# Performance work log

Hardware: AMD Instinct MI355X
Metric: run time of the kernel (lower is better)

Reference implementation:

```python
import jax, jax.numpy as jnp
import numpy as np

B, T, OB = 64, 512, 256
H = 1024
AC = 8
EPS = 1e-6


def rmsnorm(x, scale):
    # RMSNorm over the last (hidden) dim with learned scale
    return x * scale * jax.lax.rsqrt(jnp.mean(x * x, axis=-1, keepdims=True) + EPS)


def lstm_layer(x, Wih, Whh, b, gnorm, cnorm):
    """RMSNorm-gated LSTM layer. x: [B,T,in] -> [B,T,H].
    Gate pre-activations are RMSNorm'd per-gate; cell state is RMSNorm'd
    before the output tanh (the norm that breaks cuDNN gate fusion)."""
    Bsz = x.shape[0]
    Hh = Whh.shape[1]
    # precompute input projection for all timesteps: [B,T,4H]
    xp = jnp.einsum('bti,gi->btg', x, Wih) + b

    def step(carry, xpt):
        h, c = carry
        z = xpt + h @ Whh.T  # [B,4H]
        zi, zf, zg, zo = jnp.split(z, 4, axis=-1)
        i = jax.nn.sigmoid(rmsnorm(zi, gnorm[0]))
        f = jax.nn.sigmoid(rmsnorm(zf, gnorm[1]))
        g = jnp.tanh(rmsnorm(zg, gnorm[2]))
        o = jax.nn.sigmoid(rmsnorm(zo, gnorm[3]))
        c = f * c + i * g
        h = o * jnp.tanh(rmsnorm(c, cnorm))
        return (h, c), h

    init = (jnp.zeros((Bsz, Hh), x.dtype), jnp.zeros((Bsz, Hh), x.dtype))
    _, hs = jax.lax.scan(step, init, jnp.swapaxes(xp, 0, 1))  # [T,B,H]
    return jnp.swapaxes(hs, 0, 1)


def setup_inputs() -> dict:
    key = jax.random.key(0)
    ks = jax.random.split(key, 12)

    def w(k, shape, fan_in):
        return jax.random.normal(k, shape, dtype=jnp.float32) / np.sqrt(fan_in)

    return {
        'obs': jax.random.normal(ks[0], (B, T, OB), dtype=jnp.float32),
        'Wih0': w(ks[1], (4 * H, OB), OB),
        'Whh0': w(ks[2], (4 * H, H), H),
        'b0': jnp.zeros((4 * H,), jnp.float32),
        'gnorm0': jnp.ones((4, H), jnp.float32),
        'cnorm0': jnp.ones((H,), jnp.float32),
        'Wih1': w(ks[3], (4 * H, H), H),
        'Whh1': w(ks[4], (4 * H, H), H),
        'b1': jnp.zeros((4 * H,), jnp.float32),
        'gnorm1': jnp.ones((4, H), jnp.float32),
        'cnorm1': jnp.ones((H,), jnp.float32),
        'Wout': w(ks[5], (AC, H), H),
        'bout': jnp.zeros((AC,), jnp.float32),
        'std_param': jnp.zeros((AC,), jnp.float32),
    }


def reference(obs, Wih0, Whh0, b0, gnorm0, cnorm0,
              Wih1, Whh1, b1, gnorm1, cnorm1,
              Wout, bout, std_param):
    out = lstm_layer(obs, Wih0, Whh0, b0, gnorm0, cnorm0)
    out = lstm_layer(out, Wih1, Whh1, b1, gnorm1, cnorm1)
    features = out[:, -1, :]              # last timestep, like out[:, -1, :]
    mean = features @ Wout.T + bout       # [B, AC]
    std = jax.nn.softplus(std_param) + 0.01  # global learned std, [AC]
    return mean, std
```

## Files before the change

### kernel.cpp

```cpp
#include <hip/hip_runtime.h>
#include <hip/hip_bf16.h>

typedef __attribute__((ext_vector_type(8))) __bf16 bf16x8;
typedef __attribute__((ext_vector_type(4))) float f32x4;
typedef unsigned short u16;
typedef unsigned int u32;
typedef unsigned long long u64;

#define NB 64
#define NT 512
#define NH 1024
#define NOB 256
#define NWG 256
#define G4H 4096
#define BH (NB*NH)

#define S_OBS 0
#define S_H0  16384
#define S_H1  81920
#define LDS_TOTAL 147456

#define KT0 10
#define KT1 16

#define AS_RELAXED __ATOMIC_RELAXED
#define SCOPE_AGENT __HIP_MEMORY_SCOPE_AGENT
#define KEEPW(x) asm volatile("" : "+v"(x))

#define SBAR  do { asm volatile("s_barrier" ::: "memory"); __builtin_amdgcn_sched_barrier(0); } while (0)
#define LGKM0 do { asm volatile("s_waitcnt lgkmcnt(0)" ::: "memory"); __builtin_amdgcn_sched_barrier(0); } while (0)
#define VMW0  do { asm volatile("s_waitcnt vmcnt(0)" ::: "memory"); __builtin_amdgcn_sched_barrier(0); } while (0)
#define VMW8  do { asm volatile("s_waitcnt vmcnt(8)" ::: "memory"); __builtin_amdgcn_sched_barrier(0); } while (0)

__device__ __forceinline__ u16 f2bf(float f) {
  __hip_bfloat16 h = __float2bfloat16(f);
  return *reinterpret_cast<u16*>(&h);
}
__device__ __forceinline__ float sigm(float x) { return 1.f / (1.f + __expf(-x)); }
__device__ __forceinline__ float tanh_f(float x) {
  float e = __expf(2.f * x);
  return 1.f - 2.f / (e + 1.f);
}

__device__ __forceinline__ void gload_lds16(const void* g, void* l) {
  __builtin_amdgcn_global_load_lds(
      (const __attribute__((address_space(1))) void*)g,
      (__attribute__((address_space(3))) void*)l, 16, 0, 0);
}

__device__ __forceinline__ int4 load_b128_coh(const void* p) {
  int4 v;
  asm volatile("global_load_dwordx4 %0, %1, off sc0 sc1\n\ts_waitcnt vmcnt(0)"
               : "=v"(v) : "v"(p) : "memory");
  return v;
}
__device__ __forceinline__ u64 AL64(const u64* p) {
  return __hip_atomic_load(p, AS_RELAXED, SCOPE_AGENT);
}

__device__ __forceinline__ void gridbar(int* bar, int gen, bool wait) {
  __syncthreads();
  if (threadIdx.x < 64) {
    const int lane = threadIdx.x;
    if (lane == 0)
      __hip_atomic_fetch_add(&bar[(blockIdx.x & 15) * 32], 1, AS_RELAXED, SCOPE_AGENT);
    if (wait) {
      const int tgt = NWG * gen;
      for (;;) {
        int v = (lane < 16)
              ? __hip_atomic_load(&bar[lane * 32], AS_RELAXED, SCOPE_AGENT) : 0;
#pragma unroll
        for (int off = 8; off; off >>= 1) v += __shfl_xor(v, off);
        v = __shfl(v, 0);
        if (v >= tgt) break;
        __builtin_amdgcn_s_sleep(1);
      }
    }
  }
  __syncthreads();
}

__device__ __host__ __forceinline__ int wavek0(int kq, int kt) {
  return kt < 2 ? kq * 64 + kt * 32 : 256 + kq * 256 + (kt - 2) * 32;
}
__device__ __host__ __forceinline__ int wavek1(int kq, int kt) {
  return kq * 512 + kt * 32;
}

template<int LAYER>
__global__ void __launch_bounds__(256)
pack_weights(const float* __restrict__ Wih, const float* __restrict__ Whh,
             u16* __restrict__ wp) {
  constexpr int KT = LAYER ? KT1 : KT0;
  constexpr int KIN = LAYER ? 1024 : 256;
  const int total = 128 * 2 * 4 * KT * 64;
  for (int idx = blockIdx.x * blockDim.x + threadIdx.x; idx < total;
       idx += gridDim.x * blockDim.x) {
    int lane = idx & 63;
    int q = idx >> 6;
    int kt = q % KT; q /= KT;
    int kq = q & 3; q >>= 2;
    int nt = q & 1; q >>= 1;
    int slice = q;
    int outr = slice * 32 + nt * 16 + (lane & 15);
    int kb = (LAYER ? wavek1(kq, kt) : wavek0(kq, kt)) + (lane >> 4) * 8;
    union { u16 uu[8]; int4 qv; } vv;
#pragma unroll
    for (int j = 0; j < 8; ++j) {
      int k = kb + j;
      float f = (k < KIN) ? Wih[(long)outr * KIN + k] : Whh[(long)outr * NH + (k - KIN)];
      vv.uu[j] = f2bf(f);
    }
    reinterpret_cast<int4*>(wp)[idx] = vv.qv;
  }
}

__global__ void __launch_bounds__(256)
transpose_obs(const float* __restrict__ obs, u16* __restrict__ obsT) {
  long idx = (long)blockIdx.x * blockDim.x + threadIdx.x;
  if (idx >= (long)NT * NB * NOB) return;
  int k = (int)(idx & (NOB - 1));
  long r = idx >> 8;
  int b = (int)(r & (NB - 1));
  int t = (int)(r >> 6);
  obsT[idx] = f2bf(obs[((long)b * NT + t) * NOB + k]);
}

template<bool H1COH>
__global__ void __launch_bounds__(512)
fused_lstm(const u16* __restrict__ obsT,
           const u16* __restrict__ wp0, const u16* __restrict__ wp1,
           const float* __restrict__ b0, const float* __restrict__ gn0,
           const float* __restrict__ cn0,
           const float* __restrict__ b1, const float* __restrict__ gn1,
           const float* __restrict__ cn1,
           u16* __restrict__ h0hist, u16* __restrict__ h1buf, long long h1step,
           float* __restrict__ zbuf, float* __restrict__ feat,
           int* __restrict__ bar) {
  extern __shared__ char smem[];
  f32x4* sred = reinterpret_cast<f32x4*>(smem + S_H1);
  float* p2red = reinterpret_cast<float*>(smem + S_H0);

  const int tid = threadIdx.x;
  const int lane = tid & 63;
  const int wave = tid >> 6;
  const int nt = wave & 1;
  const int kq = wave >> 1;
  const int col = lane & 15;
  const int rgrp = lane >> 4;
  const int wg = blockIdx.x;
  const int bg = wg >> 7;
  const int slice = wg & 127;
  const int kl = (wave & 1) * 64 + lane;
  const int w2 = wave >> 1;

  bf16x8 wf0[KT0], wf1[KT1];
  {
    const bf16x8* p0 = reinterpret_cast<const bf16x8*>(wp0)
                     + ((size_t)((slice * 2 + nt) * 4 + kq) * KT0) * 64 + lane;
#pragma unroll
    for (int u = 0; u < KT0; ++u) { wf0[u] = p0[u * 64]; KEEPW(wf0[u]); }
    const bf16x8* p1 = reinterpret_cast<const bf16x8*>(wp1)
                     + ((size_t)((slice * 2 + nt) * 4 + kq) * KT1) * 64 + lane;
#pragma unroll
    for (int u = 0; u < KT1; ++u) { wf1[u] = p1[u * 64]; KEEPW(wf1[u]); }
  }

  const int l2 = (wg >> 6) & 1;
  const int prow = wg & 63;
  const int ej = tid * 2;
  float gn[8];
  float cw0 = 0.f, cw1 = 0.f;
  float c0 = 0.f, c1 = 0.f;
  if (wg < 128) {
    const float* gnp = l2 ? gn1 : gn0;
    const float* cnp = l2 ? cn1 : cn0;
#pragma unroll
    for (int g = 0; g < 4; ++g) {
      gn[g * 2]     = gnp[g * NH + ej];
      gn[g * 2 + 1] = gnp[g * NH + ej + 1];
    }
    cw0 = cnp[ej];
    cw1 = cnp[ej + 1];
  }
  constexpr float inv = 1.f / 1024.f;
  const bool p2wg = (wg < 128);

  {
    const u16* os = obsT + (size_t)(bg * 32) * NOB;
#pragma unroll
    for (int i = 0; i < 2; ++i) {
      const int row = 16 * i + 2 * wave + (lane >> 5);
      gload_lds16(os + (size_t)row * NOB + (size_t)(((lane & 31) ^ (row & 7)) * 8),
                  smem + S_OBS + (i * 512 + wave * 64) * 16);
    }
  }

  int gen = 0;

  for (int r = 0; r <= NT; ++r) {
    const u16* h0s = h0hist + (size_t)r * BH + (size_t)(bg * 32) * NH;
    const u16* h1s = h1buf + (size_t)r * h1step + (size_t)(bg * 32) * NH;
#pragma unroll
    for (int i = 0; i < 8; ++i) {
      const int row = i * 4 + w2;
      const int koff = (kl ^ (row & 7)) * 8;
      gload_lds16(h0s + (size_t)row * NH + koff,
                  smem + S_H0 + (i * 512 + wave * 64) * 16);
    }
    if constexpr (!H1COH) {
#pragma unroll
      for (int i = 0; i < 8; ++i) {
        const int row = i * 4 + w2;
        const int koff = (kl ^ (row & 7)) * 8;
        gload_lds16(h1s + (size_t)row * NH + koff,
                    smem + S_H1 + (i * 512 + wave * 64) * 16);
      }
      VMW8;
      SBAR;
    } else {
#pragma unroll 1
      for (int c = tid; c < 4096; c += 512) {
        int row = c >> 7, kc = c & 127;
        int4 v = load_b128_coh(h1s + (size_t)row * NH + kc * 8);
        *reinterpret_cast<int4*>(smem + S_H1 + row * 2048 + ((kc ^ (row & 7)) << 4)) = v;
      }
      VMW0; LGKM0;
      SBAR;
    }

    f32x4 a00 = {0,0,0,0}, a01 = {0,0,0,0};
    f32x4 a10 = {0,0,0,0}, a11 = {0,0,0,0};
    if (r < NT) {
#pragma unroll
      for (int kt = 0; kt < KT0; ++kt) {
        const int base   = (kt < 2) ? S_OBS : S_H0;
        const int rowstr = (kt < 2) ? 512 : 2048;
        const int chunk0 = (kt < 2) ? (kq * 8 + kt * 4) : (kq * 32 + (kt - 2) * 4);
        const int sw = (((chunk0 + rgrp) ^ (col & 7)) << 4);
        bf16x8 am0 = *reinterpret_cast<const bf16x8*>(smem + base + col * rowstr + sw);
        bf16x8 am1 = *reinterpret_cast<const bf16x8*>(smem + base + (16 + col) * rowstr + sw);
        a00 = __builtin_amdgcn_mfma_f32_16x16x32_bf16(am0, wf0[kt], a00, 0, 0, 0);
        a01 = __builtin_amdgcn_mfma_f32_16x16x32_bf16(am1, wf0[kt], a01, 0, 0, 0);
      }
    }
    if constexpr (!H1COH) {
      VMW0;
      SBAR;
    }

    if (r >= 1) {
      const int base = (kq < 2) ? S_H0 : S_H1;
#pragma unroll
      for (int kt = 0; kt < KT1; ++kt) {
        const int chunk0 = (kq & 1) * 64 + kt * 4;
        const int sw = (((chunk0 + rgrp) ^ (col & 7)) << 4);
        bf16x8 am0 = *reinterpret_cast<const bf16x8*>(smem + base + col * 2048 + sw);
        bf16x8 am1 = *reinterpret_cast<const bf16x8*>(smem + base + (16 + col) * 2048 + sw);
        a10 = __builtin_amdgcn_mfma_f32_16x16x32_bf16(am0, wf1[kt], a10, 0, 0, 0);
        a11 = __builtin_amdgcn_mfma_f32_16x16x32_bf16(am1, wf1[kt], a11, 0, 0, 0);
      }
    }
    LGKM0;
    SBAR;

    {
      f32x4* pw = sred + wave * 512 + lane;
      pw[0 * 64] = a00;
      pw[1 * 64] = a01;
      pw[2 * 64] = a10;
      pw[3 * 64] = a11;
    }
    LGKM0;
    SBAR;
    {
      const int q = tid >> 6, ln = tid & 63;
      const int fcol = ln & 15, frg = ln >> 4;
      const int lm = q & 3;
      const int nq2 = q >> 2;
      f32x4 s = sred[(nq2 + 0) * 512 + lm * 64 + ln]
              + sred[(nq2 + 2) * 512 + lm * 64 + ln]
              + sred[(nq2 + 4) * 512 + lm * 64 + ln]
              + sred[(nq2 + 6) * 512 + lm * 64 + ln];
      const int l = lm >> 1, m = lm & 1;
      const bool zv = l ? (r >= 1) : (r < NT);
      if (zv) {
        const int outg = slice * 32 + nq2 * 16 + fcol;
        const float bv = (l ? b1 : b0)[outg];
        float* zr = zbuf + ((size_t)l * NB + bg * 32 + m * 16 + frg * 4) * G4H + outg;
#pragma unroll
        for (int j = 0; j < 4; ++j)
          __hip_atomic_store(&zr[(size_t)j * G4H], s[j] + bv, AS_RELAXED, SCOPE_AGENT);
      }
    }
    gridbar(bar, ++gen, p2wg);

    if (r + 1 < NT) {
      const u16* os = obsT + (size_t)(r + 1) * (NB * NOB) + (size_t)(bg * 32) * NOB;
#pragma unroll
      for (int i = 0; i < 2; ++i) {
        const int row = 16 * i + 2 * wave + (lane >> 5);
        gload_lds16(os + (size_t)row * NOB + (size_t)(((lane & 31) ^ (row & 7)) * 8),
                    smem + S_OBS + (i * 512 + wave * 64) * 16);
      }
    }

    if (p2wg && (l2 ? (r >= 1) : (r < NT))) {
      const u64* zq = reinterpret_cast<const u64*>(
          zbuf + ((size_t)l2 * NB + prow) * G4H);
      union { u64 q; float f[2]; } va, vb, vg, vo;
      va.q = AL64(zq + tid);
      vb.q = AL64(zq + 512 + tid);
      vg.q = AL64(zq + 1024 + tid);
      vo.q = AL64(zq + 1536 + tid);
      float s0 = va.f[0] * va.f[0] + va.f[1] * va.f[1];
      float s1 = vb.f[0] * vb.f[0] + vb.f[1] * vb.f[1];
      float s2 = vg.f[0] * vg.f[0] + vg.f[1] * vg.f[1];
      float s3 = vo.f[0] * vo.f[0] + vo.f[1] * vo.f[1];
#pragma unroll
      for (int off = 32; off; off >>= 1) {
        s0 += __shfl_xor(s0, off);
        s1 += __shfl_xor(s1, off);
        s2 += __shfl_xor(s2, off);
        s3 += __shfl_xor(s3, off);
      }
      if (lane == 0) {
        float* sp = p2red + wave * 4;
        sp[0] = s0; sp[1] = s1; sp[2] = s2; sp[3] = s3;
      }
      __syncthreads();
      float t0 = 0.f, t1 = 0.f, t2 = 0.f, t3 = 0.f;
#pragma unroll
      for (int w = 0; w < 8; ++w) {
        t0 += p2red[w * 4 + 0]; t1 += p2red[w * 4 + 1];
        t2 += p2red[w * 4 + 2]; t3 += p2red[w * 4 + 3];
      }
      const float r0 = rsqrtf(t0 * inv + 1e-6f);
      const float r1 = rsqrtf(t1 * inv + 1e-6f);
      const float r2 = rsqrtf(t2 * inv + 1e-6f);
      const float r3 = rsqrtf(t3 * inv + 1e-6f);
      const float i0 = sigm(va.f[0] * gn[0] * r0), i1 = sigm(va.f[1] * gn[1] * r0);
      const float f0 = sigm(vb.f[0] * gn[2] * r1), f1 = sigm(vb.f[1] * gn[3] * r1);
      const float g0 = tanh_f(vg.f[0] * gn[4] * r2), g1 = tanh_f(vg.f[1] * gn[5] * r2);
      const float o0 = sigm(vo.f[0] * gn[6] * r3), o1 = sigm(vo.f[1] * gn[7] * r3);
      c0 = f0 * c0 + i0 * g0;
      c1 = f1 * c1 + i1 * g1;
      float cs = c0 * c0 + c1 * c1;
#pragma unroll
      for (int off = 32; off; off >>= 1) cs += __shfl_xor(cs, off);
      if (lane == 0) p2red[32 + wave] = cs;
      __syncthreads();
      float ct = 0.f;
#pragma unroll
      for (int w = 0; w < 8; ++w) ct += p2red[32 + w];
      const float rc = rsqrtf(ct * inv + 1e-6f);
      const float hx = o0 * tanh_f(c0 * cw0 * rc);
      const float hy = o1 * tanh_f(c1 * cw1 * rc);
      u16* hw;
      if (l2 == 0) hw = h0hist + (size_t)(r + 1) * BH + (size_t)prow * NH + ej;
      else         hw = h1buf + (size_t)(r + 1) * h1step + (size_t)prow * NH + ej;
      const u32 packed = (u32)f2bf(hx) | ((u32)f2bf(hy) << 16);
      __hip_atomic_store(reinterpret_cast<u32*>(hw), packed, AS_RELAXED, SCOPE_AGENT);
      if (l2 == 1 && r == NT) {
        feat[(size_t)prow * NH + ej] = hx;
        feat[(size_t)prow * NH + ej + 1] = hy;
      }
    }
    gridbar(bar, ++gen, true);
  }
}

__global__ void __launch_bounds__(256)
head_kernel(const float* __restrict__ feat, const float* __restrict__ Wout,
            const float* __restrict__ bout, const float* __restrict__ stdp,
            float* __restrict__ out) {
  int b = blockIdx.x;
  int a = threadIdx.x >> 5;
  int l = threadIdx.x & 31;
  float s = 0.f;
  for (int k = l; k < NH; k += 32) s += feat[b * NH + k] * Wout[a * NH + k];
#pragma unroll
  for (int off = 16; off; off >>= 1) s += __shfl_xor(s, off, 32);
  if (l == 0) out[b * 8 + a] = s + bout[a];
  if (b == 0 && threadIdx.x < 8) {
    float x = stdp[threadIdx.x];
    float splus = (x > 20.f) ? x : log1pf(__expf(x));
    out[512 + threadIdx.x] = splus + 0.01f;
  }
}

extern "C" void kernel_launch(void* const* d_in, const int* in_sizes, int n_in,
                              void* d_out, int out_size, void* d_ws, size_t ws_size,
                              hipStream_t stream) {
  (void)in_sizes; (void)n_in; (void)out_size;
  const float* obs  = (const float*)d_in[0];
  const float* Wih0 = (const float*)d_in[1];
  const float* Whh0 = (const float*)d_in[2];
  const float* b0   = (const float*)d_in[3];
  const float* gn0  = (const float*)d_in[4];
  const float* cn0  = (const float*)d_in[5];
  const float* Wih1 = (const float*)d_in[6];
  const float* Whh1 = (const float*)d_in[7];
  const float* b1   = (const float*)d_in[8];
  const float* gn1  = (const float*)d_in[9];
  const float* cn1  = (const float*)d_in[10];
  const float* Wout = (const float*)d_in[11];
  const float* bout = (const float*)d_in[12];
  const float* stdp = (const float*)d_in[13];
  float* out = (float*)d_out;

  char* ws = (char*)d_ws;
  size_t off = 0;
  auto take = [&](size_t bytes) -> char* {
    char* p = ws + off;
    off = (off + bytes + 255) & ~(size_t)255;
    return p;
  };

  const size_t WP0_B  = (size_t)128 * 2 * 4 * KT0 * 64 * 16;
  const size_t WP1_B  = (size_t)128 * 2 * 4 * KT1 * 64 * 16;
  const size_t OBST_B = (size_t)NT * NB * NOB * 2;
  const size_t H0H_B  = (size_t)(NT + 1) * BH * 2;
  const size_t H1H_B  = (size_t)(NT + 2) * BH * 2;

  u16* wp0    = (u16*)take(WP0_B);
  u16* wp1    = (u16*)take(WP1_B);
  u16* obsT   = (u16*)take(OBST_B);
  u16* h0hist = (u16*)take(H0H_B);
  u16* h1b    = (u16*)take(H1H_B);
  float* zbuf = (float*)take((size_t)2 * NB * G4H * 4);
  float* feat = (float*)take((size_t)NB * NH * 4);
  int* bars   = (int*)take(4096);
  bool fits = (off <= ws_size);
  long long h1step = BH;

  if (!fits) {
    off = 0;
    wp0    = (u16*)take(WP0_B);
    wp1    = (u16*)take(WP1_B);
    obsT   = (u16*)take(OBST_B);
    h0hist = (u16*)take(H0H_B);
    h1b    = (u16*)take((size_t)BH * 2);
    zbuf   = (float*)take((size_t)2 * NB * G4H * 4);
    feat   = (float*)take((size_t)NB * NH * 4);
    bars   = (int*)take(4096);
    h1step = 0;
    if (off > ws_size) return;
  }

  (void)hipFuncSetAttribute((const void*)fused_lstm<false>,
                            hipFuncAttributeMaxDynamicSharedMemorySize, LDS_TOTAL);
  (void)hipFuncSetAttribute((const void*)fused_lstm<true>,
                            hipFuncAttributeMaxDynamicSharedMemorySize, LDS_TOTAL);

  hipMemsetAsync(bars, 0, 4096, stream);
  hipMemsetAsync(h0hist, 0, (size_t)BH * 2, stream);
  hipMemsetAsync(h1b, 0, (size_t)(fits ? 2 : 1) * BH * 2, stream);

  pack_weights<0><<<2560, 256, 0, stream>>>(Wih0, Whh0, wp0);
  pack_weights<1><<<4096, 256, 0, stream>>>(Wih1, Whh1, wp1);
  transpose_obs<<<(NT * NB * NOB) / 256, 256, 0, stream>>>(obs, obsT);

  if (fits) {
    fused_lstm<false><<<NWG, 512, LDS_TOTAL, stream>>>(
        obsT, wp0, wp1, b0, gn0, cn0, b1, gn1, cn1,
        h0hist, h1b, h1step, zbuf, feat, bars);
  } else {
    fused_lstm<true><<<NWG, 512, LDS_TOTAL, stream>>>(
        obsT, wp0, wp1, b0, gn0, cn0, b1, gn1, cn1,
        h0hist, h1b, 0LL, zbuf, feat, bars);
  }

  head_kernel<<<NB, 256, 0, stream>>>(feat, Wout, bout, stdp, out);
}
```

Before: 6.455 ms.

## Split layer phases into half-steps with dedicated pointwise wave and per-batch-group barriers

The fused persistent LSTM loop is restructured into alternating half-steps: even half-steps run layer-0 GEMMs and layer-1 pointwise, odd half-steps run layer-1 GEMMs and layer-0 pointwise. A ninth wave per workgroup does the RMSNorm/gate pointwise work on 16 elements per lane, and the grid barrier is split per batch group (128 WGs each). This aims to remove the second grid barrier per step and overlap pointwise work with MFMA work. It doubles the number of loop iterations and removes the fallback path for small workspaces.

Measured after the change: 17.97 ms. 2.78x slower.

```diff
diff --git a/kernel.cpp b/kernel.cpp
--- a/kernel.cpp
+++ b/kernel.cpp
@@ -3,6 +3,7 @@
 
 typedef __attribute__((ext_vector_type(8))) __bf16 bf16x8;
 typedef __attribute__((ext_vector_type(4))) float f32x4;
+typedef __attribute__((ext_vector_type(4))) int i32x4;
 typedef unsigned short u16;
 typedef unsigned int u32;
 typedef unsigned long long u64;
@@ -12,13 +13,15 @@
 #define NH 1024
 #define NOB 256
 #define NWG 256
+#define HALF_WG 128
 #define G4H 4096
 #define BH (NB*NH)
 
 #define S_OBS 0
 #define S_H0  16384
 #define S_H1  81920
-#define LDS_TOTAL 147456
+#define S_RED 147456
+#define LDS_TOTAL 163840
 
 #define KT0 10
 #define KT1 16
@@ -30,7 +33,7 @@
 #define SBAR  do { asm volatile("s_barrier" ::: "memory"); __builtin_amdgcn_sched_barrier(0); } while (0)
 #define LGKM0 do { asm volatile("s_waitcnt lgkmcnt(0)" ::: "memory"); __builtin_amdgcn_sched_barrier(0); } while (0)
 #define VMW0  do { asm volatile("s_waitcnt vmcnt(0)" ::: "memory"); __builtin_amdgcn_sched_barrier(0); } while (0)
-#define VMW8  do { asm volatile("s_waitcnt vmcnt(8)" ::: "memory"); __builtin_amdgcn_sched_barrier(0); } while (0)
+#define VMW2  do { asm volatile("s_waitcnt vmcnt(2)" ::: "memory"); __builtin_amdgcn_sched_barrier(0); } while (0)
 
 __device__ __forceinline__ u16 f2bf(float f) {
   __hip_bfloat16 h = __float2bfloat16(f);
@@ -47,34 +50,28 @@
       (const __attribute__((address_space(1))) void*)g,
       (__attribute__((address_space(3))) void*)l, 16, 0, 0);
 }
-
-__device__ __forceinline__ int4 load_b128_coh(const void* p) {
-  int4 v;
-  asm volatile("global_load_dwordx4 %0, %1, off sc0 sc1\n\ts_waitcnt vmcnt(0)"
-               : "=v"(v) : "v"(p) : "memory");
-  return v;
-}
-__device__ __forceinline__ u64 AL64(const u64* p) {
-  return __hip_atomic_load(p, AS_RELAXED, SCOPE_AGENT);
-}
-
-__device__ __forceinline__ void gridbar(int* bar, int gen, bool wait) {
+__device__ __forceinline__ void ld16a(i32x4& d, const void* p) {
+  asm volatile("global_load_dwordx4 %0, %1, off sc0 sc1" : "=v"(d) : "v"(p));
+}
+__device__ __forceinline__ void st16c(void* p, i32x4 v) {
+  asm volatile("global_store_dwordx4 %0, %1, off sc0 sc1" :: "v"(p), "v"(v) : "memory");
+}
+
+__device__ __forceinline__ void gridbar(int* barD, int myleaf, int gen) {
   __syncthreads();
   if (threadIdx.x < 64) {
     const int lane = threadIdx.x;
     if (lane == 0)
-      __hip_atomic_fetch_add(&bar[(blockIdx.x & 15) * 32], 1, AS_RELAXED, SCOPE_AGENT);
-    if (wait) {
-      const int tgt = NWG * gen;
-      for (;;) {
-        int v = (lane < 16)
-              ? __hip_atomic_load(&bar[lane * 32], AS_RELAXED, SCOPE_AGENT) : 0;
-#pragma unroll
-        for (int off = 8; off; off >>= 1) v += __shfl_xor(v, off);
-        v = __shfl(v, 0);
-        if (v >= tgt) break;
-        __builtin_amdgcn_s_sleep(1);
-      }
+      __hip_atomic_fetch_add(&barD[myleaf * 32], 1, AS_RELAXED, SCOPE_AGENT);
+    const int tgt = HALF_WG * gen;
+    for (;;) {
+      int v = (lane < 16)
+            ? __hip_atomic_load(&barD[lane * 32], AS_RELAXED, SCOPE_AGENT) : 0;
+#pragma unroll
+      for (int off = 8; off; off >>= 1) v += __shfl_xor(v, off);
+      v = __shfl(v, 0);
+      if (v >= tgt) break;
+      __builtin_amdgcn_s_sleep(1);
     }
   }
   __syncthreads();
@@ -126,20 +123,18 @@
   obsT[idx] = f2bf(obs[((long)b * NT + t) * NOB + k]);
 }
 
-template<bool H1COH>
-__global__ void __launch_bounds__(512)
+__global__ void __launch_bounds__(576)
 fused_lstm(const u16* __restrict__ obsT,
            const u16* __restrict__ wp0, const u16* __restrict__ wp1,
            const float* __restrict__ b0, const float* __restrict__ gn0,
            const float* __restrict__ cn0,
            const float* __restrict__ b1, const float* __restrict__ gn1,
            const float* __restrict__ cn1,
-           u16* __restrict__ h0hist, u16* __restrict__ h1buf, long long h1step,
+           u16* __restrict__ h0hist, u16* __restrict__ h1buf,
            float* __restrict__ zbuf, float* __restrict__ feat,
            int* __restrict__ bar) {
   extern __shared__ char smem[];
-  f32x4* sred = reinterpret_cast<f32x4*>(smem + S_H1);
-  float* p2red = reinterpret_cast<float*>(smem + S_H0);
+  f32x4* sredp = reinterpret_cast<f32x4*>(smem + S_RED);
 
   const int tid = threadIdx.x;
   const int lane = tid & 63;
@@ -153,9 +148,13 @@
   const int slice = wg & 127;
   const int kl = (wave & 1) * 64 + lane;
   const int w2 = wave >> 1;
+  float* z0 = zbuf;
+  float* z1 = zbuf + (size_t)NB * G4H;
+  int* barD = bar + bg * 512;
+  const int myleaf = slice & 15;
 
   bf16x8 wf0[KT0], wf1[KT1];
-  {
+  if (wave < 8) {
     const bf16x8* p0 = reinterpret_cast<const bf16x8*>(wp0)
                      + ((size_t)((slice * 2 + nt) * 4 + kq) * KT0) * 64 + lane;
 #pragma unroll
@@ -166,27 +165,23 @@
     for (int u = 0; u < KT1; ++u) { wf1[u] = p1[u * 64]; KEEPW(wf1[u]); }
   }
 
-  const int l2 = (wg >> 6) & 1;
-  const int prow = wg & 63;
-  const int ej = tid * 2;
-  float gn[8];
-  float cw0 = 0.f, cw1 = 0.f;
-  float c0 = 0.f, c1 = 0.f;
-  if (wg < 128) {
-    const float* gnp = l2 ? gn1 : gn0;
-    const float* cnp = l2 ? cn1 : cn0;
-#pragma unroll
-    for (int g = 0; g < 4; ++g) {
-      gn[g * 2]     = gnp[g * NH + ej];
-      gn[g * 2 + 1] = gnp[g * NH + ej + 1];
-    }
-    cw0 = cnp[ej];
-    cw1 = cnp[ej + 1];
+  const int pl = lane;
+  const int pLayer = (slice >= 32) ? 1 : 0;
+  const int prow2 = bg * 32 + (slice & 31);
+  float pgn[4][16], pcw[16], pc[16];
+  if (wave == 8 && slice < 64) {
+    const float* gnp = pLayer ? gn1 : gn0;
+    const float* cnp = pLayer ? cn1 : cn0;
+#pragma unroll
+    for (int g = 0; g < 4; ++g)
+#pragma unroll
+      for (int k = 0; k < 16; ++k) pgn[g][k] = gnp[g * NH + pl * 16 + k];
+#pragma unroll
+    for (int k = 0; k < 16; ++k) { pcw[k] = cnp[pl * 16 + k]; pc[k] = 0.f; }
   }
   constexpr float inv = 1.f / 1024.f;
-  const bool p2wg = (wg < 128);
-
-  {
+
+  if (wave < 8) {
     const u16* os = obsT + (size_t)(bg * 32) * NOB;
 #pragma unroll
     for (int i = 0; i < 2; ++i) {
@@ -196,177 +191,178 @@
     }
   }
 
-  int gen = 0;
-
-  for (int r = 0; r <= NT; ++r) {
-    const u16* h0s = h0hist + (size_t)r * BH + (size_t)(bg * 32) * NH;
-    const u16* h1s = h1buf + (size_t)r * h1step + (size_t)(bg * 32) * NH;
-#pragma unroll
-    for (int i = 0; i < 8; ++i) {
-      const int row = i * 4 + w2;
-      const int koff = (kl ^ (row & 7)) * 8;
-      gload_lds16(h0s + (size_t)row * NH + koff,
-                  smem + S_H0 + (i * 512 + wave * 64) * 16);
-    }
-    if constexpr (!H1COH) {
-#pragma unroll
-      for (int i = 0; i < 8; ++i) {
-        const int row = i * 4 + w2;
-        const int koff = (kl ^ (row & 7)) * 8;
-        gload_lds16(h1s + (size_t)row * NH + koff,
-                    smem + S_H1 + (i * 512 + wave * 64) * 16);
-      }
-      VMW8;
-      SBAR;
-    } else {
-#pragma unroll 1
-      for (int c = tid; c < 4096; c += 512) {
-        int row = c >> 7, kc = c & 127;
-        int4 v = load_b128_coh(h1s + (size_t)row * NH + kc * 8);
-        *reinterpret_cast<int4*>(smem + S_H1 + row * 2048 + ((kc ^ (row & 7)) << 4)) = v;
-      }
-      VMW0; LGKM0;
-      SBAR;
-    }
-
-    f32x4 a00 = {0,0,0,0}, a01 = {0,0,0,0};
-    f32x4 a10 = {0,0,0,0}, a11 = {0,0,0,0};
-    if (r < NT) {
-#pragma unroll
-      for (int kt = 0; kt < KT0; ++kt) {
-        const int base   = (kt < 2) ? S_OBS : S_H0;
-        const int rowstr = (kt < 2) ? 512 : 2048;
-        const int chunk0 = (kt < 2) ? (kq * 8 + kt * 4) : (kq * 32 + (kt - 2) * 4);
-        const int sw = (((chunk0 + rgrp) ^ (col & 7)) << 4);
-        bf16x8 am0 = *reinterpret_cast<const bf16x8*>(smem + base + col * rowstr + sw);
-        bf16x8 am1 = *reinterpret_cast<const bf16x8*>(smem + base + (16 + col) * rowstr + sw);
-        a00 = __builtin_amdgcn_mfma_f32_16x16x32_bf16(am0, wf0[kt], a00, 0, 0, 0);
-        a01 = __builtin_amdgcn_mfma_f32_16x16x32_bf16(am1, wf0[kt], a01, 0, 0, 0);
-      }
-    }
-    if constexpr (!H1COH) {
+  for (int t = 0; t <= 2 * NT + 2; ++t) {
+    const int r = t >> 1;
+    const int odd = t & 1;
+    bool obsIssued = false;
+
+    if (wave < 8) {
+      if (!odd) {
+        if (r <= NT) {
+          const u16* h0s = h0hist + (size_t)r * BH + (size_t)(bg * 32) * NH;
+#pragma unroll
+          for (int i = 0; i < 8; ++i) {
+            const int row = i * 4 + w2;
+            const int koff = (kl ^ (row & 7)) * 8;
+            gload_lds16(h0s + (size_t)row * NH + koff,
+                        smem + S_H0 + (i * 512 + wave * 64) * 16);
+          }
+        }
+      } else {
+        if (r >= 1 && r <= NT) {
+          const u16* h1s = h1buf + (size_t)r * BH + (size_t)(bg * 32) * NH;
+#pragma unroll
+          for (int i = 0; i < 8; ++i) {
+            const int row = i * 4 + w2;
+            const int koff = (kl ^ (row & 7)) * 8;
+            gload_lds16(h1s + (size_t)row * NH + koff,
+                        smem + S_H1 + (i * 512 + wave * 64) * 16);
+          }
+        }
+        if (r + 1 < NT) {
+          obsIssued = true;
+          const u16* os = obsT + (size_t)(r + 1) * (NB * NOB) + (size_t)(bg * 32) * NOB;
+#pragma unroll
+          for (int i = 0; i < 2; ++i) {
+            const int row = 16 * i + 2 * wave + (lane >> 5);
+            gload_lds16(os + (size_t)row * NOB + (size_t)(((lane & 31) ^ (row & 7)) * 8),
+                        smem + S_OBS + (i * 512 + wave * 64) * 16);
+          }
+        }
+      }
+    }
+    if (obsIssued) { VMW2; } else { VMW0; }
+    SBAR;
+
+    f32x4 a0 = {0.f, 0.f, 0.f, 0.f}, a1 = {0.f, 0.f, 0.f, 0.f};
+    const bool p2act = (wave == 8) && (slice < 64) &&
+        (odd ? (pLayer == 0 && r <= NT - 1)
+             : (pLayer == 1 && r >= 2 && r <= NT + 1));
+    i32x4 zr4[4][4];
+    float rs0 = 0.f, rs1 = 0.f, rs2 = 0.f, rs3 = 0.f;
+
+    if (wave < 8) {
+      if (!odd) {
+        if (r < NT) {
+#pragma unroll
+          for (int kt = 0; kt < KT0; ++kt) {
+            const int base   = (kt < 2) ? S_OBS : S_H0;
+            const int rowstr = (kt < 2) ? 512 : 2048;
+            const int chunk0 = (kt < 2) ? (kq * 8 + kt * 4) : (kq * 32 + (kt - 2) * 4);
+            const int sw = (((chunk0 + rgrp) ^ (col & 7)) << 4);
+            bf16x8 am0 = *reinterpret_cast<const bf16x8*>(smem + base + col * rowstr + sw);
+            bf16x8 am1 = *reinterpret_cast<const bf16x8*>(smem + base + (16 + col) * rowstr + sw);
+            a0 = __builtin_amdgcn_mfma_f32_16x16x32_bf16(am0, wf0[kt], a0, 0, 0, 0);
+            a1 = __builtin_amdgcn_mfma_f32_16x16x32_bf16(am1, wf0[kt], a1, 0, 0, 0);
+          }
+        }
+      } else {
+        if (r >= 1 && r <= NT) {
+          const int base = (kq < 2) ? S_H0 : S_H1;
+#pragma unroll
+          for (int kt = 0; kt < KT1; ++kt) {
+            const int chunk0 = (kq & 1) * 64 + kt * 4;
+            const int sw = (((chunk0 + rgrp) ^ (col & 7)) << 4);
+            bf16x8 am0 = *reinterpret_cast<const bf16x8*>(smem + base + col * 2048 + sw);
+            bf16x8 am1 = *reinterpret_cast<const bf16x8*>(smem + base + (16 + col) * 2048 + sw);
+            a0 = __builtin_amdgcn_mfma_f32_16x16x32_bf16(am0, wf1[kt], a0, 0, 0, 0);
+            a1 = __builtin_amdgcn_mfma_f32_16x16x32_bf16(am1, wf1[kt], a1, 0, 0, 0);
+          }
+        }
+      }
+      f32x4* pw = sredp + wave * 128 + lane;
+      pw[0]  = a0;
+      pw[64] = a1;
+    } else if (p2act) {
+      const float* zrow = (odd ? z0 : z1) + (size_t)prow2 * G4H;
+#pragma unroll
+      for (int g = 0; g < 4; ++g)
+#pragma unroll
+        for (int c4 = 0; c4 < 4; ++c4)
+          ld16a(zr4[g][c4],
+                reinterpret_cast<const char*>(zrow) + (size_t)(g * NH + pl * 16 + c4 * 4) * 4);
       VMW0;
-      SBAR;
-    }
-
-    if (r >= 1) {
-      const int base = (kq < 2) ? S_H0 : S_H1;
-#pragma unroll
-      for (int kt = 0; kt < KT1; ++kt) {
-        const int chunk0 = (kq & 1) * 64 + kt * 4;
-        const int sw = (((chunk0 + rgrp) ^ (col & 7)) << 4);
-        bf16x8 am0 = *reinterpret_cast<const bf16x8*>(smem + base + col * 2048 + sw);
-        bf16x8 am1 = *reinterpret_cast<const bf16x8*>(smem + base + (16 + col) * 2048 + sw);
-        a10 = __builtin_amdgcn_mfma_f32_16x16x32_bf16(am0, wf1[kt], a10, 0, 0, 0);
-        a11 = __builtin_amdgcn_mfma_f32_16x16x32_bf16(am1, wf1[kt], a11, 0, 0, 0);
-      }
+      float sq[4];
+#pragma unroll
+      for (int g = 0; g < 4; ++g) {
+        float s = 0.f;
+#pragma unroll
+        for (int c4 = 0; c4 < 4; ++c4)
+#pragma unroll
+          for (int e = 0; e < 4; ++e) {
+            float v = reinterpret_cast<const float*>(&zr4[g][c4])[e];
+            s += v * v;
+          }
+        sq[g] = s;
+      }
+#pragma unroll
+      for (int off = 32; off; off >>= 1) {
+        sq[0] += __shfl_xor(sq[0], off);
+        sq[1] += __shfl_xor(sq[1], off);
+        sq[2] += __shfl_xor(sq[2], off);
+        sq[3] += __shfl_xor(sq[3], off);
+      }
+      rs0 = rsqrtf(sq[0] * inv + 1e-6f);
+      rs1 = rsqrtf(sq[1] * inv + 1e-6f);
+      rs2 = rsqrtf(sq[2] * inv + 1e-6f);
+      rs3 = rsqrtf(sq[3] * inv + 1e-6f);
     }
     LGKM0;
     SBAR;
 
-    {
-      f32x4* pw = sred + wave * 512 + lane;
-      pw[0 * 64] = a00;
-      pw[1 * 64] = a01;
-      pw[2 * 64] = a10;
-      pw[3 * 64] = a11;
-    }
-    LGKM0;
-    SBAR;
-    {
-      const int q = tid >> 6, ln = tid & 63;
-      const int fcol = ln & 15, frg = ln >> 4;
-      const int lm = q & 3;
-      const int nq2 = q >> 2;
-      f32x4 s = sred[(nq2 + 0) * 512 + lm * 64 + ln]
-              + sred[(nq2 + 2) * 512 + lm * 64 + ln]
-              + sred[(nq2 + 4) * 512 + lm * 64 + ln]
-              + sred[(nq2 + 6) * 512 + lm * 64 + ln];
-      const int l = lm >> 1, m = lm & 1;
-      const bool zv = l ? (r >= 1) : (r < NT);
+    if (wave < 4) {
+      const int rnt = wave & 1, rm = wave >> 1;
+      const int fcol = lane & 15, frg = lane >> 4;
+      f32x4 s = sredp[(0 + rnt) * 128 + rm * 64 + lane]
+              + sredp[(2 + rnt) * 128 + rm * 64 + lane]
+              + sredp[(4 + rnt) * 128 + rm * 64 + lane]
+              + sredp[(6 + rnt) * 128 + rm * 64 + lane];
+      const bool zv = odd ? (r >= 1 && r <= NT) : (r < NT);
       if (zv) {
-        const int outg = slice * 32 + nq2 * 16 + fcol;
-        const float bv = (l ? b1 : b0)[outg];
-        float* zr = zbuf + ((size_t)l * NB + bg * 32 + m * 16 + frg * 4) * G4H + outg;
+        const int outg = slice * 32 + rnt * 16 + fcol;
+        const float bv = (odd ? b1 : b0)[outg];
+        float* zr = (odd ? z1 : z0) + ((size_t)(bg * 32 + rm * 16 + frg * 4)) * G4H + outg;
 #pragma unroll
         for (int j = 0; j < 4; ++j)
           __hip_atomic_store(&zr[(size_t)j * G4H], s[j] + bv, AS_RELAXED, SCOPE_AGENT);
       }
-    }
-    gridbar(bar, ++gen, p2wg);
-
-    if (r + 1 < NT) {
-      const u16* os = obsT + (size_t)(r + 1) * (NB * NOB) + (size_t)(bg * 32) * NOB;
-#pragma unroll
-      for (int i = 0; i < 2; ++i) {
-        const int row = 16 * i + 2 * wave + (lane >> 5);
-        gload_lds16(os + (size_t)row * NOB + (size_t)(((lane & 31) ^ (row & 7)) * 8),
-                    smem + S_OBS + (i * 512 + wave * 64) * 16);
-      }
-    }
-
-    if (p2wg && (l2 ? (r >= 1) : (r < NT))) {
-      const u64* zq = reinterpret_cast<const u64*>(
-          zbuf + ((size_t)l2 * NB + prow) * G4H);
-      union { u64 q; float f[2]; } va, vb, vg, vo;
-      va.q = AL64(zq + tid);
-      vb.q = AL64(zq + 512 + tid);
-      vg.q = AL64(zq + 1024 + tid);
-      vo.q = AL64(zq + 1536 + tid);
-      float s0 = va.f[0] * va.f[0] + va.f[1] * va.f[1];
-      float s1 = vb.f[0] * vb.f[0] + vb.f[1] * vb.f[1];
-      float s2 = vg.f[0] * vg.f[0] + vg.f[1] * vg.f[1];
-      float s3 = vo.f[0] * vo.f[0] + vo.f[1] * vo.f[1];
-#pragma unroll
-      for (int off = 32; off; off >>= 1) {
-        s0 += __shfl_xor(s0, off);
-        s1 += __shfl_xor(s1, off);
-        s2 += __shfl_xor(s2, off);
-        s3 += __shfl_xor(s3, off);
-      }
-      if (lane == 0) {
-        float* sp = p2red + wave * 4;
-        sp[0] = s0; sp[1] = s1; sp[2] = s2; sp[3] = s3;
-      }
-      __syncthreads();
-      float t0 = 0.f, t1 = 0.f, t2 = 0.f, t3 = 0.f;
-#pragma unroll
-      for (int w = 0; w < 8; ++w) {
-        t0 += p2red[w * 4 + 0]; t1 += p2red[w * 4 + 1];
-        t2 += p2red[w * 4 + 2]; t3 += p2red[w * 4 + 3];
-      }
-      const float r0 = rsqrtf(t0 * inv + 1e-6f);
-      const float r1 = rsqrtf(t1 * inv + 1e-6f);
-      const float r2 = rsqrtf(t2 * inv + 1e-6f);
-      const float r3 = rsqrtf(t3 * inv + 1e-6f);
-      const float i0 = sigm(va.f[0] * gn[0] * r0), i1 = sigm(va.f[1] * gn[1] * r0);
-      const float f0 = sigm(vb.f[0] * gn[2] * r1), f1 = sigm(vb.f[1] * gn[3] * r1);
-      const float g0 = tanh_f(vg.f[0] * gn[4] * r2), g1 = tanh_f(vg.f[1] * gn[5] * r2);
-      const float o0 = sigm(vo.f[0] * gn[6] * r3), o1 = sigm(vo.f[1] * gn[7] * r3);
-      c0 = f0 * c0 + i0 * g0;
-      c1 = f1 * c1 + i1 * g1;
-      float cs = c0 * c0 + c1 * c1;
+    } else if (p2act) {
+      float ovv[16];
+      float cs = 0.f;
+#pragma unroll
+      for (int k = 0; k < 16; ++k) {
+        const float zi = reinterpret_cast<const float*>(&zr4[0][k >> 2])[k & 3];
+        const float zf = reinterpret_cast<const float*>(&zr4[1][k >> 2])[k & 3];
+        const float zg = reinterpret_cast<const float*>(&zr4[2][k >> 2])[k & 3];
+        const float zo = reinterpret_cast<const float*>(&zr4[3][k >> 2])[k & 3];
+        const float iv = sigm(zi * pgn[0][k] * rs0);
+        const float fv = sigm(zf * pgn[1][k] * rs1);
+        const float gv = tanh_f(zg * pgn[2][k] * rs2);
+        ovv[k] = sigm(zo * pgn[3][k] * rs3);
+        pc[k] = fv * pc[k] + iv * gv;
+        cs += pc[k] * pc[k];
+      }
 #pragma unroll
       for (int off = 32; off; off >>= 1) cs += __shfl_xor(cs, off);
-      if (lane == 0) p2red[32 + wave] = cs;
-      __syncthreads();
-      float ct = 0.f;
-#pragma unroll
-      for (int w = 0; w < 8; ++w) ct += p2red[32 + w];
-      const float rc = rsqrtf(ct * inv + 1e-6f);
-      const float hx = o0 * tanh_f(c0 * cw0 * rc);
-      const float hy = o1 * tanh_f(c1 * cw1 * rc);
-      u16* hw;
-      if (l2 == 0) hw = h0hist + (size_t)(r + 1) * BH + (size_t)prow * NH + ej;
-      else         hw = h1buf + (size_t)(r + 1) * h1step + (size_t)prow * NH + ej;
-      const u32 packed = (u32)f2bf(hx) | ((u32)f2bf(hy) << 16);
-      __hip_atomic_store(reinterpret_cast<u32*>(hw), packed, AS_RELAXED, SCOPE_AGENT);
-      if (l2 == 1 && r == NT) {
-        feat[(size_t)prow * NH + ej] = hx;
-        feat[(size_t)prow * NH + ej + 1] = hy;
-      }
-    }
-    gridbar(bar, ++gen, true);
+      const float rc = rsqrtf(cs * inv + 1e-6f);
+      float hv[16];
+      union { u16 uu[16]; i32x4 q[2]; } hp;
+#pragma unroll
+      for (int k = 0; k < 16; ++k) {
+        hv[k] = ovv[k] * tanh_f(pc[k] * pcw[k] * rc);
+        hp.uu[k] = f2bf(hv[k]);
+      }
+      u16* hd = (odd ? h0hist + (size_t)(r + 1) * BH : h1buf + (size_t)r * BH)
+              + (size_t)prow2 * NH + pl * 16;
+      st16c(hd, hp.q[0]);
+      st16c(hd + 8, hp.q[1]);
+      if (!odd && r == NT + 1) {
+        float* fd = feat + (size_t)prow2 * NH + pl * 16;
+#pragma unroll
+        for (int k = 0; k < 16; ++k) fd[k] = hv[k];
+      }
+    }
+    gridbar(barD, myleaf, t + 1);
   }
 }
 
@@ -431,45 +427,22 @@
   float* zbuf = (float*)take((size_t)2 * NB * G4H * 4);
   float* feat = (float*)take((size_t)NB * NH * 4);
   int* bars   = (int*)take(4096);
-  bool fits = (off <= ws_size);
-  long long h1step = BH;
-
-  if (!fits) {
-    off = 0;
-    wp0    = (u16*)take(WP0_B);
-    wp1    = (u16*)take(WP1_B);
-    obsT   = (u16*)take(OBST_B);
-    h0hist = (u16*)take(H0H_B);
-    h1b    = (u16*)take((size_t)BH * 2);
-    zbuf   = (float*)take((size_t)2 * NB * G4H * 4);
-    feat   = (float*)take((size_t)NB * NH * 4);
-    bars   = (int*)take(4096);
-    h1step = 0;
-    if (off > ws_size) return;
-  }
-
-  (void)hipFuncSetAttribute((const void*)fused_lstm<false>,
+  if (off > ws_size) return;
+
+  (void)hipFuncSetAttribute((const void*)fused_lstm,
                             hipFuncAttributeMaxDynamicSharedMemorySize, LDS_TOTAL);
-  (void)hipFuncSetAttribute((const void*)fused_lstm<true>,
-                            hipFuncAttributeMaxDynamicSharedMemorySize, LDS_TOTAL);
-
-  hipMemsetAsync(bars, 0, 4096, stream);
-  hipMemsetAsync(h0hist, 0, (size_t)BH * 2, stream);
-  hipMemsetAsync(h1b, 0, (size_t)(fits ? 2 : 1) * BH * 2, stream);
+
+  (void)hipMemsetAsync(bars, 0, 4096, stream);
+  (void)hipMemsetAsync(h0hist, 0, (size_t)BH * 2, stream);
+  (void)hipMemsetAsync(h1b, 0, (size_t)2 * BH * 2, stream);
 
   pack_weights<0><<<2560, 256, 0, stream>>>(Wih0, Whh0, wp0);
   pack_weights<1><<<4096, 256, 0, stream>>>(Wih1, Whh1, wp1);
   transpose_obs<<<(NT * NB * NOB) / 256, 256, 0, stream>>>(obs, obsT);
 
-  if (fits) {
-    fused_lstm<false><<<NWG, 512, LDS_TOTAL, stream>>>(
-        obsT, wp0, wp1, b0, gn0, cn0, b1, gn1, cn1,
-        h0hist, h1b, h1step, zbuf, feat, bars);
-  } else {
-    fused_lstm<true><<<NWG, 512, LDS_TOTAL, stream>>>(
-        obsT, wp0, wp1, b0, gn0, cn0, b1, gn1, cn1,
-        h0hist, h1b, 0LL, zbuf, feat, bars);
-  }
+  fused_lstm<<<NWG, 576, LDS_TOTAL, stream>>>(
+      obsT, wp0, wp1, b0, gn0, cn0, b1, gn1, cn1,
+      h0hist, h1b, zbuf, feat, bars);
 
   head_kernel<<<NB, 256, 0, stream>>>(feat, Wout, bout, stdp, out);
 }
```

## Split grid barrier into two independent per-batch-group barriers

Applied to the files above, without the earlier changes.

The persistent kernel's grid-wide barrier is replaced by two independent barriers, one per batch group of 128 workgroups. The pointwise (phase-2) work is remapped so each batch group handles its own 32 rows for both layers. Each group then synchronizes only with itself, which cuts barrier contention and waiting on the slower half. Every workgroup now waits at both barriers, including ones that previously skipped the first wait, and the barrier buffer is enlarged.

Result: faster. 5.209 ms, median of 2 (-19.3%).

```diff
diff --git a/kernel.cpp b/kernel.cpp
--- a/kernel.cpp
+++ b/kernel.cpp
@@ -12,6 +12,7 @@
 #define NH 1024
 #define NOB 256
 #define NWG 256
+#define HALF_WG 128
 #define G4H 4096
 #define BH (NB*NH)
 
@@ -58,23 +59,21 @@
   return __hip_atomic_load(p, AS_RELAXED, SCOPE_AGENT);
 }
 
-__device__ __forceinline__ void gridbar(int* bar, int gen, bool wait) {
+__device__ __forceinline__ void gridbar(int* barD, int myleaf, int gen) {
   __syncthreads();
   if (threadIdx.x < 64) {
     const int lane = threadIdx.x;
     if (lane == 0)
-      __hip_atomic_fetch_add(&bar[(blockIdx.x & 15) * 32], 1, AS_RELAXED, SCOPE_AGENT);
-    if (wait) {
-      const int tgt = NWG * gen;
-      for (;;) {
-        int v = (lane < 16)
-              ? __hip_atomic_load(&bar[lane * 32], AS_RELAXED, SCOPE_AGENT) : 0;
-#pragma unroll
-        for (int off = 8; off; off >>= 1) v += __shfl_xor(v, off);
-        v = __shfl(v, 0);
-        if (v >= tgt) break;
-        __builtin_amdgcn_s_sleep(1);
-      }
+      __hip_atomic_fetch_add(&barD[myleaf * 32], 1, AS_RELAXED, SCOPE_AGENT);
+    const int tgt = HALF_WG * gen;
+    for (;;) {
+      int v = (lane < 16)
+            ? __hip_atomic_load(&barD[lane * 32], AS_RELAXED, SCOPE_AGENT) : 0;
+#pragma unroll
+      for (int off = 8; off; off >>= 1) v += __shfl_xor(v, off);
+      v = __shfl(v, 0);
+      if (v >= tgt) break;
+      __builtin_amdgcn_s_sleep(1);
     }
   }
   __syncthreads();
@@ -153,6 +152,8 @@
   const int slice = wg & 127;
   const int kl = (wave & 1) * 64 + lane;
   const int w2 = wave >> 1;
+  int* barD = bar + bg * 512;
+  const int myleaf = slice & 15;
 
   bf16x8 wf0[KT0], wf1[KT1];
   {
@@ -166,13 +167,14 @@
     for (int u = 0; u < KT1; ++u) { wf1[u] = p1[u * 64]; KEEPW(wf1[u]); }
   }
 
-  const int l2 = (wg >> 6) & 1;
-  const int prow = wg & 63;
+  const bool p2wg = (slice < 64);
+  const int l2 = (slice >> 5) & 1;
+  const int prow = bg * 32 + (slice & 31);
   const int ej = tid * 2;
   float gn[8];
   float cw0 = 0.f, cw1 = 0.f;
   float c0 = 0.f, c1 = 0.f;
-  if (wg < 128) {
+  if (p2wg) {
     const float* gnp = l2 ? gn1 : gn0;
     const float* cnp = l2 ? cn1 : cn0;
 #pragma unroll
@@ -184,7 +186,6 @@
     cw1 = cnp[ej + 1];
   }
   constexpr float inv = 1.f / 1024.f;
-  const bool p2wg = (wg < 128);
 
   {
     const u16* os = obsT + (size_t)(bg * 32) * NOB;
@@ -293,7 +294,7 @@
           __hip_atomic_store(&zr[(size_t)j * G4H], s[j] + bv, AS_RELAXED, SCOPE_AGENT);
       }
     }
-    gridbar(bar, ++gen, p2wg);
+    gridbar(barD, myleaf, ++gen);
 
     if (r + 1 < NT) {
       const u16* os = obsT + (size_t)(r + 1) * (NB * NOB) + (size_t)(bg * 32) * NOB;
@@ -366,7 +367,7 @@
         feat[(size_t)prow * NH + ej + 1] = hy;
       }
     }
-    gridbar(bar, ++gen, true);
+    gridbar(barD, myleaf, ++gen);
   }
 }
 
@@ -430,7 +431,7 @@
   u16* h1b    = (u16*)take(H1H_B);
   float* zbuf = (float*)take((size_t)2 * NB * G4H * 4);
   float* feat = (float*)take((size_t)NB * NH * 4);
-  int* bars   = (int*)take(4096);
+  int* bars   = (int*)take(8192);
   bool fits = (off <= ws_size);
   long long h1step = BH;
 
@@ -443,7 +444,7 @@
     h1b    = (u16*)take((size_t)BH * 2);
     zbuf   = (float*)take((size_t)2 * NB * G4H * 4);
     feat   = (float*)take((size_t)NB * NH * 4);
-    bars   = (int*)take(4096);
+    bars   = (int*)take(8192);
     h1step = 0;
     if (off > ws_size) return;
   }
@@ -453,9 +454,9 @@
   (void)hipFuncSetAttribute((const void*)fused_lstm<true>,
                             hipFuncAttributeMaxDynamicSharedMemorySize, LDS_TOTAL);
 
-  hipMemsetAsync(bars, 0, 4096, stream);
-  hipMemsetAsync(h0hist, 0, (size_t)BH * 2, stream);
-  hipMemsetAsync(h1b, 0, (size_t)(fits ? 2 : 1) * BH * 2, stream);
+  (void)hipMemsetAsync(bars, 0, 8192, stream);
+  (void)hipMemsetAsync(h0hist, 0, (size_t)BH * 2, stream);
+  (void)hipMemsetAsync(h1b, 0, (size_t)(fits ? 2 : 1) * BH * 2, stream);
 
   pack_weights<0><<<2560, 256, 0, stream>>>(Wih0, Whh0, wp0);
   pack_weights<1><<<4096, 256, 0, stream>>>(Wih1, Whh1, wp1);
```
